# Kernel tuning notes

Measured on AMD Instinct MI355X. Metric: run time of the kernel, lower is better.

## Reference

```python
import jax, jax.numpy as jnp
import numpy as np

SHIFT_MIN, SHIFT_MAX = -14.0, 0.0  # weight_bits=5 -> (-(2^4-2), 0)
FRAC_BITS = 16
INT_BITS = 16


def round_to_fixed(x):
    # deepshift utils.round_to_fixed: floor to 2^-16 grid, clamp to [-2^15, 2^15-1]
    delta = 2.0 ** (-FRAC_BITS)
    bound = 2.0 ** (INT_BITS - 1)
    r = jnp.floor(x / delta) * delta
    return jnp.clip(r, -bound, bound - 1)


def setup_inputs() -> dict:
    key = jax.random.key(0)
    k1, k2, k3, k4 = jax.random.split(key, 4)
    N, IN, OUT = 524288, 128, 128
    x = jax.random.normal(k1, (N, IN), dtype=jnp.float32)
    shift = jax.random.uniform(k2, (OUT, IN), dtype=jnp.float32, minval=SHIFT_MIN, maxval=SHIFT_MAX)
    sign = jax.random.uniform(k3, (OUT, IN), dtype=jnp.float32, minval=-1.0, maxval=1.0)
    bound = 1.0 / np.sqrt(IN)
    bias = jax.random.uniform(k4, (OUT,), dtype=jnp.float32, minval=-bound, maxval=bound)
    return {"input": x, "shift": shift, "sign": sign, "bias": bias}


def reference(input, shift, sign, bias):
    # quantize weights: v = 2^round(clamp(shift)) * sign(round(sign))
    shift_r = jnp.round(jnp.clip(shift, SHIFT_MIN, SHIFT_MAX))
    sign_s = jnp.sign(jnp.round(sign))
    v = jnp.exp2(shift_r) * sign_s  # [OUT, IN]
    x_q = round_to_fixed(input)
    b_q = round_to_fixed(bias)
    # F.linear: x @ v.T + b
    return jnp.dot(x_q, v.T) + b_q[None, :]
```

## Files before the change

kernel.cpp:

```cpp
#include <hip/hip_runtime.h>
#include <hip/hip_bf16.h>

typedef __attribute__((ext_vector_type(4))) float f32x4;
typedef __attribute__((ext_vector_type(8))) short bf16x8;

constexpr int IN_DIM  = 128;
constexpr int OUT_DIM = 128;
constexpr int BLOCK   = 512;
constexpr int WAVES   = 8;
constexpr int CHUNKS  = 4;
constexpr int CHUNK_ROWS = WAVES * 16;
constexpr int ROWS_PER_BLOCK = CHUNK_ROWS * CHUNKS;

__global__ __launch_bounds__(BLOCK, 4)
void linshift_kernel(const float* __restrict__ x,
                     const float* __restrict__ shiftp,
                     const float* __restrict__ signp,
                     const float* __restrict__ biasp,
                     float* __restrict__ out)
{
    __shared__ ushort v_lds[16 * OUT_DIM * 8];
    __shared__ float  b_lds[OUT_DIM];

    const int t = threadIdx.x;

    #pragma unroll
    for (int s = 0; s < (OUT_DIM * IN_DIM / 8) / BLOCK; ++s) {
        const int seg = t + s * BLOCK;
        const int row = seg >> 4;
        const int j   = seg & 15;
        const int g   = row * IN_DIM + j * 8;
        f32x4 sh0 = *reinterpret_cast<const f32x4*>(shiftp + g);
        f32x4 sh1 = *reinterpret_cast<const f32x4*>(shiftp + g + 4);
        f32x4 sg0 = *reinterpret_cast<const f32x4*>(signp + g);
        f32x4 sg1 = *reinterpret_cast<const f32x4*>(signp + g + 4);
        union { ushort u[8]; bf16x8 v; } tmp;
        #pragma unroll
        for (int e = 0; e < 8; ++e) {
            float sh = (e < 4) ? sh0[e] : sh1[e - 4];
            float sg = (e < 4) ? sg0[e] : sg1[e - 4];
            sh = fminf(fmaxf(sh, -14.0f), 0.0f);
            const int   si = (int)rintf(sh);
            const float rs = rintf(sg);
            ushort bits = 0;
            if (rs != 0.0f)
                bits = (ushort)(((rs < 0.0f) ? 0x8000u : 0u) |
                                (unsigned)((127 + si) << 7));
            tmp.u[e] = bits;
        }
        *reinterpret_cast<bf16x8*>(&v_lds[(j * OUT_DIM + row) * 8]) = tmp.v;
    }
    if (t < OUT_DIM)
        b_lds[t] = floorf(biasp[t] * 65536.0f) * (1.0f / 65536.0f);
    __syncthreads();

    const int wave = t >> 6;
    const int lane = t & 63;
    const int rl = lane & 15;
    const int kb = lane >> 4;

    const long long row0 = (long long)blockIdx.x * ROWS_PER_BLOCK + wave * 16 + rl;
    const float* xp = x + row0 * IN_DIM + kb * 8;
    float* op0 = out + row0 * OUT_DIM;

    f32x4 f[8];
    #pragma unroll
    for (int ks = 0; ks < 4; ++ks) {
        f[2 * ks]     = *reinterpret_cast<const f32x4*>(xp + ks * 32);
        f[2 * ks + 1] = *reinterpret_cast<const f32x4*>(xp + ks * 32 + 4);
    }

    #pragma unroll
    for (int c = 0; c < CHUNKS; ++c) {
        f32x4 fn[8];
        if (c + 1 < CHUNKS) {
            const float* xq = xp + (long long)(c + 1) * CHUNK_ROWS * IN_DIM;
            #pragma unroll
            for (int ks = 0; ks < 4; ++ks) {
                fn[2 * ks]     = *reinterpret_cast<const f32x4*>(xq + ks * 32);
                fn[2 * ks + 1] = *reinterpret_cast<const f32x4*>(xq + ks * 32 + 4);
            }
        }

        bf16x8 xb[4];
        #pragma unroll
        for (int ks = 0; ks < 4; ++ks) {
            union { ushort u[8]; bf16x8 v; } tmp;
            #pragma unroll
            for (int e = 0; e < 4; ++e) {
                __hip_bfloat16 h0 = __float2bfloat16(f[2 * ks][e]);
                __hip_bfloat16 h1 = __float2bfloat16(f[2 * ks + 1][e]);
                tmp.u[e]     = *reinterpret_cast<const ushort*>(&h0);
                tmp.u[e + 4] = *reinterpret_cast<const ushort*>(&h1);
            }
            xb[ks] = tmp.v;
        }

        float* op = op0 + (long long)c * CHUNK_ROWS * OUT_DIM;
        #pragma unroll
        for (int ct = 0; ct < 8; ++ct) {
            f32x4 acc = {0.f, 0.f, 0.f, 0.f};
            #pragma unroll
            for (int ks = 0; ks < 4; ++ks) {
                const int kidx = ks * 4 + kb;
                bf16x8 vb = *reinterpret_cast<const bf16x8*>(
                    &v_lds[(kidx * OUT_DIM + ct * 16 + rl) * 8]);
                acc = __builtin_amdgcn_mfma_f32_16x16x32_bf16(vb, xb[ks], acc, 0, 0, 0);
            }
            f32x4 bv = *reinterpret_cast<const f32x4*>(&b_lds[ct * 16 + kb * 4]);
            f32x4 o = acc + bv;
            *reinterpret_cast<f32x4*>(op + ct * 16 + kb * 4) = o;
        }

        #pragma unroll
        for (int i = 0; i < 8; ++i) f[i] = fn[i];
    }
}

extern "C" void kernel_launch(void* const* d_in, const int* in_sizes, int n_in,
                              void* d_out, int out_size, void* d_ws, size_t ws_size,
                              hipStream_t stream) {
    const float* x  = (const float*)d_in[0];
    const float* sh = (const float*)d_in[1];
    const float* sg = (const float*)d_in[2];
    const float* b  = (const float*)d_in[3];
    float* out = (float*)d_out;

    const int N = in_sizes[0] / IN_DIM;
    const int grid = N / ROWS_PER_BLOCK;
    linshift_kernel<<<grid, BLOCK, 0, stream>>>(x, sh, sg, b, out);
}
```

Baseline: 116.9 us.

## Precompute quantized weights in a prep kernel and switch to 32x32 MFMA tiles

Adds a small build kernel that quantizes shift/sign into bf16 power-of-two weights in workspace once, so each main block only copies them into LDS instead of recomputing them. The main kernel moves to 256-thread blocks of 128 rows, uses 32x32x16 bf16 MFMA with the bias preloaded into the accumulator, and drops the multi-chunk software prefetch of x. This cuts the per-block weight-build overhead and the LDS B-fragment reads per MFMA. In exchange it adds a second launch, gives up the x-load prefetch overlap, and writes output as scalar strided stores instead of float4 stores.

```diff
diff --git a/kernel.cpp b/kernel.cpp
--- a/kernel.cpp
+++ b/kernel.cpp
@@ -1,119 +1,140 @@
 #include <hip/hip_runtime.h>
 #include <hip/hip_bf16.h>
 
-typedef __attribute__((ext_vector_type(4))) float f32x4;
-typedef __attribute__((ext_vector_type(8))) short bf16x8;
+typedef __attribute__((ext_vector_type(4)))  float f32x4;
+typedef __attribute__((ext_vector_type(16))) float f32x16;
+typedef __attribute__((ext_vector_type(8)))  short bf16x8;
 
 constexpr int IN_DIM  = 128;
 constexpr int OUT_DIM = 128;
-constexpr int BLOCK   = 512;
-constexpr int WAVES   = 8;
-constexpr int CHUNKS  = 4;
-constexpr int CHUNK_ROWS = WAVES * 16;
-constexpr int ROWS_PER_BLOCK = CHUNK_ROWS * CHUNKS;
+constexpr int BLOCK   = 256;
+constexpr int ROWS_PER_BLOCK = 4 * 32;
+constexpr size_t WS_V_BYTES = 16 * 128 * 8 * sizeof(ushort);
+constexpr size_t WS_NEED    = WS_V_BYTES + 128 * sizeof(float);
 
+__device__ inline bf16x8 build_seg(const float* __restrict__ shiftp,
+                                   const float* __restrict__ signp,
+                                   int row, int j)
+{
+    const int g = row * IN_DIM + j * 8;
+    f32x4 sh0 = *reinterpret_cast<const f32x4*>(shiftp + g);
+    f32x4 sh1 = *reinterpret_cast<const f32x4*>(shiftp + g + 4);
+    f32x4 sg0 = *reinterpret_cast<const f32x4*>(signp + g);
+    f32x4 sg1 = *reinterpret_cast<const f32x4*>(signp + g + 4);
+    union { ushort u[8]; bf16x8 v; } tmp;
+    #pragma unroll
+    for (int e = 0; e < 8; ++e) {
+        float sh = (e < 4) ? sh0[e] : sh1[e - 4];
+        float sg = (e < 4) ? sg0[e] : sg1[e - 4];
+        sh = fminf(fmaxf(sh, -14.0f), 0.0f);
+        const int   si = (int)rintf(sh);
+        const float rs = rintf(sg);
+        ushort bits = 0;
+        if (rs != 0.0f)
+            bits = (ushort)(((rs < 0.0f) ? 0x8000u : 0u) |
+                            (unsigned)((127 + si) << 7));
+        tmp.u[e] = bits;
+    }
+    return tmp.v;
+}
+
+__global__ void build_kernel(const float* __restrict__ shiftp,
+                             const float* __restrict__ signp,
+                             const float* __restrict__ biasp,
+                             ushort* __restrict__ wsv, float* __restrict__ wsb)
+{
+    const int seg = blockIdx.x * 256 + threadIdx.x;
+    const int row = seg >> 4;
+    const int j   = seg & 15;
+    bf16x8 v = build_seg(shiftp, signp, row, j);
+    *reinterpret_cast<bf16x8*>(&wsv[(j * OUT_DIM + row) * 8]) = v;
+    if (blockIdx.x == 0 && threadIdx.x < OUT_DIM)
+        wsb[threadIdx.x] = floorf(biasp[threadIdx.x] * 65536.0f) * (1.0f / 65536.0f);
+}
+
+template<bool PRE>
 __global__ __launch_bounds__(BLOCK, 4)
-void linshift_kernel(const float* __restrict__ x,
-                     const float* __restrict__ shiftp,
-                     const float* __restrict__ signp,
-                     const float* __restrict__ biasp,
-                     float* __restrict__ out)
+void linshift_main(const float* __restrict__ x,
+                   const float* __restrict__ shiftp,
+                   const float* __restrict__ signp,
+                   const float* __restrict__ biasp,
+                   const ushort* __restrict__ wsv,
+                   const float* __restrict__ wsb,
+                   float* __restrict__ out)
 {
     __shared__ ushort v_lds[16 * OUT_DIM * 8];
     __shared__ float  b_lds[OUT_DIM];
 
     const int t = threadIdx.x;
-
-    #pragma unroll
-    for (int s = 0; s < (OUT_DIM * IN_DIM / 8) / BLOCK; ++s) {
-        const int seg = t + s * BLOCK;
-        const int row = seg >> 4;
-        const int j   = seg & 15;
-        const int g   = row * IN_DIM + j * 8;
-        f32x4 sh0 = *reinterpret_cast<const f32x4*>(shiftp + g);
-        f32x4 sh1 = *reinterpret_cast<const f32x4*>(shiftp + g + 4);
-        f32x4 sg0 = *reinterpret_cast<const f32x4*>(signp + g);
-        f32x4 sg1 = *reinterpret_cast<const f32x4*>(signp + g + 4);
-        union { ushort u[8]; bf16x8 v; } tmp;
+    if (PRE) {
+        const f32x4* src = reinterpret_cast<const f32x4*>(wsv);
+        f32x4*       dst = reinterpret_cast<f32x4*>(v_lds);
         #pragma unroll
-        for (int e = 0; e < 8; ++e) {
-            float sh = (e < 4) ? sh0[e] : sh1[e - 4];
-            float sg = (e < 4) ? sg0[e] : sg1[e - 4];
-            sh = fminf(fmaxf(sh, -14.0f), 0.0f);
-            const int   si = (int)rintf(sh);
-            const float rs = rintf(sg);
-            ushort bits = 0;
-            if (rs != 0.0f)
-                bits = (ushort)(((rs < 0.0f) ? 0x8000u : 0u) |
-                                (unsigned)((127 + si) << 7));
-            tmp.u[e] = bits;
+        for (int i = 0; i < 8; ++i) dst[t + i * 256] = src[t + i * 256];
+        if (t < OUT_DIM) b_lds[t] = wsb[t];
+    } else {
+        #pragma unroll
+        for (int s = 0; s < 8; ++s) {
+            const int seg = t + s * 256;
+            const int row = seg >> 4, j = seg & 15;
+            bf16x8 v = build_seg(shiftp, signp, row, j);
+            *reinterpret_cast<bf16x8*>(&v_lds[(j * OUT_DIM + row) * 8]) = v;
         }
-        *reinterpret_cast<bf16x8*>(&v_lds[(j * OUT_DIM + row) * 8]) = tmp.v;
+        if (t < OUT_DIM) b_lds[t] = floorf(biasp[t] * 65536.0f) * (1.0f / 65536.0f);
     }
-    if (t < OUT_DIM)
-        b_lds[t] = floorf(biasp[t] * 65536.0f) * (1.0f / 65536.0f);
     __syncthreads();
 
-    const int wave = t >> 6;
-    const int lane = t & 63;
-    const int rl = lane & 15;
-    const int kb = lane >> 4;
+    const int wave = t >> 6, lane = t & 63;
+    const int ml = lane & 31;
+    const int hi = lane >> 5;
 
-    const long long row0 = (long long)blockIdx.x * ROWS_PER_BLOCK + wave * 16 + rl;
-    const float* xp = x + row0 * IN_DIM + kb * 8;
-    float* op0 = out + row0 * OUT_DIM;
+    const long long row0 = (long long)blockIdx.x * ROWS_PER_BLOCK + wave * 32;
+    const float* xp = x + (row0 + ml) * IN_DIM + hi * 8;
 
-    f32x4 f[8];
+    bf16x8 a[8];
     #pragma unroll
-    for (int ks = 0; ks < 4; ++ks) {
-        f[2 * ks]     = *reinterpret_cast<const f32x4*>(xp + ks * 32);
-        f[2 * ks + 1] = *reinterpret_cast<const f32x4*>(xp + ks * 32 + 4);
-    }
-
-    #pragma unroll
-    for (int c = 0; c < CHUNKS; ++c) {
-        f32x4 fn[8];
-        if (c + 1 < CHUNKS) {
-            const float* xq = xp + (long long)(c + 1) * CHUNK_ROWS * IN_DIM;
-            #pragma unroll
-            for (int ks = 0; ks < 4; ++ks) {
-                fn[2 * ks]     = *reinterpret_cast<const f32x4*>(xq + ks * 32);
-                fn[2 * ks + 1] = *reinterpret_cast<const f32x4*>(xq + ks * 32 + 4);
-            }
+    for (int half = 0; half < 2; ++half) {
+        f32x4 f[8];
+        #pragma unroll
+        for (int q = 0; q < 4; ++q) {
+            const int ks = half * 4 + q;
+            f[2 * q]     = *reinterpret_cast<const f32x4*>(xp + ks * 16);
+            f[2 * q + 1] = *reinterpret_cast<const f32x4*>(xp + ks * 16 + 4);
         }
-
-        bf16x8 xb[4];
         #pragma unroll
-        for (int ks = 0; ks < 4; ++ks) {
+        for (int q = 0; q < 4; ++q) {
             union { ushort u[8]; bf16x8 v; } tmp;
             #pragma unroll
             for (int e = 0; e < 4; ++e) {
-                __hip_bfloat16 h0 = __float2bfloat16(f[2 * ks][e]);
-                __hip_bfloat16 h1 = __float2bfloat16(f[2 * ks + 1][e]);
+                __hip_bfloat16 h0 = __float2bfloat16(f[2 * q][e]);
+                __hip_bfloat16 h1 = __float2bfloat16(f[2 * q + 1][e]);
                 tmp.u[e]     = *reinterpret_cast<const ushort*>(&h0);
                 tmp.u[e + 4] = *reinterpret_cast<const ushort*>(&h1);
             }
-            xb[ks] = tmp.v;
+            a[half * 4 + q] = tmp.v;
         }
+    }
 
-        float* op = op0 + (long long)c * CHUNK_ROWS * OUT_DIM;
+    float* op = out + row0 * OUT_DIM;
+    #pragma unroll
+    for (int ct = 0; ct < 4; ++ct) {
+        const float bv = b_lds[ct * 32 + ml];
+        f32x16 acc;
         #pragma unroll
-        for (int ct = 0; ct < 8; ++ct) {
-            f32x4 acc = {0.f, 0.f, 0.f, 0.f};
-            #pragma unroll
-            for (int ks = 0; ks < 4; ++ks) {
-                const int kidx = ks * 4 + kb;
-                bf16x8 vb = *reinterpret_cast<const bf16x8*>(
-                    &v_lds[(kidx * OUT_DIM + ct * 16 + rl) * 8]);
-                acc = __builtin_amdgcn_mfma_f32_16x16x32_bf16(vb, xb[ks], acc, 0, 0, 0);
-            }
-            f32x4 bv = *reinterpret_cast<const f32x4*>(&b_lds[ct * 16 + kb * 4]);
-            f32x4 o = acc + bv;
-            *reinterpret_cast<f32x4*>(op + ct * 16 + kb * 4) = o;
+        for (int r = 0; r < 16; ++r) acc[r] = bv;
+
+        #pragma unroll
+        for (int ks = 0; ks < 8; ++ks) {
+            bf16x8 vb = *reinterpret_cast<const bf16x8*>(
+                &v_lds[((ks * 2 + hi) * OUT_DIM + ct * 32 + ml) * 8]);
+            acc = __builtin_amdgcn_mfma_f32_32x32x16_bf16(a[ks], vb, acc, 0, 0, 0);
         }
 
         #pragma unroll
-        for (int i = 0; i < 8; ++i) f[i] = fn[i];
+        for (int r = 0; r < 16; ++r) {
+            const int m = (r & 3) + 8 * (r >> 2) + 4 * hi;
+            op[(long long)m * OUT_DIM + ct * 32 + ml] = acc[r];
+        }
     }
 }
 
@@ -128,5 +149,14 @@
 
     const int N = in_sizes[0] / IN_DIM;
     const int grid = N / ROWS_PER_BLOCK;
-    linshift_kernel<<<grid, BLOCK, 0, stream>>>(x, sh, sg, b, out);
+
+    if (ws_size >= WS_NEED) {
+        ushort* wsv = (ushort*)d_ws;
+        float*  wsb = (float*)((char*)d_ws + WS_V_BYTES);
+        build_kernel<<<8, 256, 0, stream>>>(sh, sg, b, wsv, wsb);
+        linshift_main<true><<<grid, BLOCK, 0, stream>>>(x, sh, sg, b, wsv, wsb, out);
+    } else {
+        linshift_main<false><<<grid, BLOCK, 0, stream>>>(x, sh, sg, b,
+                                                         nullptr, nullptr, out);
+    }
 }
```

Measured after the change: 121.9 us. 4.3% more time.
